# Kernel optimization log

Measured on AMD Instinct MI355X. Metric: run time of the kernel, lower is better.

Reference implementation:

```python
import itertools
import jax, jax.numpy as jnp
import numpy as np

ALPHA = 1e-4   # mse/conn mixing
BETA = 0.1
DMAX = 20.0
NCAP = 10.0    # costs_n_cap
PCAP = 3.0     # costs_p_cap
W3D = 64       # 3D cube window (window_3d)
W2D = 32       # 2D MALIS window (window_2d, default)


def _dilate5(mask):
    # scipy binary_dilation, default cross structuring element, 5 iterations
    m = mask.astype(bool)
    for _ in range(5):
        p = np.pad(m, 1)
        m = p[1:-1, 1:-1] | p[:-2, 1:-1] | p[2:, 1:-1] | p[1:-1, :-2] | p[1:-1, 2:]
    return m


def _label8(mask):
    # skimage.measure.label on boolean mask: 8-connectivity, background=0
    H, W = mask.shape
    lbl = np.zeros((H, W), np.int64)
    parent = {}

    def find(x):
        while parent[x] != x:
            parent[x] = parent[parent[x]]
            x = parent[x]
        return x

    nxt = 1
    for i in range(H):
        for j in range(W):
            if not mask[i, j]:
                continue
            neigh = []
            for di, dj in ((-1, -1), (-1, 0), (-1, 1), (0, -1)):
                ii, jj = i + di, j + dj
                if 0 <= ii < H and 0 <= jj < W and mask[ii, jj]:
                    neigh.append(int(lbl[ii, jj]))
            if not neigh:
                lbl[i, j] = nxt
                parent[nxt] = nxt
                nxt += 1
            else:
                m0 = min(neigh)
                lbl[i, j] = m0
                for nb in neigh:
                    ra, rb = find(m0), find(nb)
                    if ra != rb:
                        parent[max(ra, rb)] = min(ra, rb)
    out = np.zeros_like(lbl)
    remap = {}
    c = 0
    for i in range(H):
        for j in range(W):
            if lbl[i, j] > 0:
                r = find(int(lbl[i, j]))
                if r not in remap:
                    c += 1
                    remap[r] = c
                out[i, j] = remap[r]
    return out


def _malis_edge_weights(seg, n1, n2, costs, pos):
    # MALIS union-find / Kruskal maximal-spanning-tree pair counting.
    # Edges processed in descending cost order. Background (seg==0) nodes
    # are not counted. pos=1: #same-label pairs merged; pos=0: #diff-label pairs.
    n = seg.size
    parent = list(range(n))

    def find(x):
        r = x
        while parent[r] != r:
            r = parent[r]
        while parent[x] != r:
            parent[x], x = r, parent[x]
        return r

    cnt = [({int(s): 1} if s > 0 else {}) for s in seg]
    tot = [1 if s > 0 else 0 for s in seg]
    w = np.zeros(costs.shape[0], np.float32)
    for e in np.argsort(-costs, kind="stable"):
        ra, rb = find(int(n1[e])), find(int(n2[e]))
        if ra == rb:
            continue
        ca, cb = cnt[ra], cnt[rb]
        if len(ca) > len(cb):
            ra, rb, ca, cb = rb, ra, cb, ca
        same = 0
        for l, v in ca.items():
            same += v * cb.get(l, 0)
        w[e] = float(same if pos else tot[ra] * tot[rb] - same)
        for l, v in ca.items():
            cb[l] = cb.get(l, 0) + v
        tot[rb] += tot[ra]
        parent[ra] = rb
        cnt[ra] = None
    return w


def _window_weights(pred2d, tgt2d):
    # numpy MALIS node weights for a [B,1,H,W] 2D projection
    B, C, H, W = pred2d.shape
    w = W2D
    wn = np.zeros(pred2d.shape, np.float32)
    wp = np.zeros(pred2d.shape, np.float32)
    idx = np.arange(w * w).reshape(w, w)
    n1 = np.concatenate([idx[:, :-1].ravel(), idx[:-1, :].ravel()])
    n2 = np.concatenate([idx[:, 1:].ravel(), idx[1:, :].ravel()])
    nh = w * (w - 1)
    for k in range(H // w):
        for j in range(W // w):
            p = pred2d[:, :, k*w:(k+1)*w, j*w:(j+1)*w]
            t = tgt2d[:, :, k*w:(k+1)*w, j*w:(j+1)*w]
            ch = (p[:, :, :, :-1] + p[:, :, :, 1:]).reshape(B, -1)
            cv = (p[:, :, :-1, :] + p[:, :, 1:, :]).reshape(B, -1)
            costs = np.concatenate([ch, cv], 1).astype(np.float32)
            gh = (t[:, :, :, :-1] + t[:, :, :, 1:]).reshape(B, -1)
            gv = (t[:, :, :-1, :] + t[:, :, 1:, :]).reshape(B, -1)
            gt = np.concatenate([gh, gv], 1).astype(np.float32)
            costs_n = costs.copy()
            costs_p = costs.copy()
            costs_n[gt > NCAP] = NCAP
            costs_p[gt < PCAP] = 0.0
            gt = np.minimum(gt, NCAP)
            for b in range(B):
                sg = _label8(~_dilate5(t[b, 0] == 0)).ravel()
                en = _malis_edge_weights(sg, n1, n2, costs_n[b], 0)
                ep = _malis_edge_weights(sg, n1, n2, costs_p[b], 1)
                sn = en.sum()
                if sn > 0:
                    en = en / sn
                sp = ep.sum()
                if sp > 0:
                    ep = ep / sp
                en[gt[b] >= PCAP] = 0.0
                ep[gt[b] < NCAP] = 0.0
                for ew, out in ((en, wn), (ep, wp)):
                    eh = ew[:nh].reshape(w, w - 1)
                    ev = ew[nh:].reshape(w - 1, w)
                    nwt = np.zeros((w, w), np.float32)
                    nwt[:, :-1] += eh
                    nwt[:, 1:] += eh
                    nwt[:-1, :] += ev
                    nwt[1:, :] += ev
                    out[b, 0, k*w:(k+1)*w, j*w:(j+1)*w] = nwt
    return wn, wp


def _precompute(pred_np, tgt_np):
    # host-side (detached) MALIS weight maps, exactly as the torch module
    B, C, H, W, D = pred_np.shape
    items = []
    for k, j, i in itertools.product(range(H // W3D), range(W // W3D), range(D // W3D)):
        sl = (slice(None), slice(None), slice(k*W3D, (k+1)*W3D),
              slice(j*W3D, (j+1)*W3D), slice(i*W3D, (i+1)*W3D))
        pc, tc = pred_np[sl], tgt_np[sl]
        for axis in (2, 3, 4):
            wn, wp = _window_weights(pc.min(axis=axis), tc.min(axis=axis))
            items.append((k, j, i, axis, jnp.asarray(wn), jnp.asarray(wp)))
    return items


def _loss(pred, target, items):
    mse = jnp.mean((pred - target) ** 2)
    conn = jnp.float32(0.0)
    for (k, j, i, axis, wn, wp) in items:
        pc = pred[:, :, k*W3D:(k+1)*W3D, j*W3D:(j+1)*W3D, i*W3D:(i+1)*W3D]
        proj = jnp.min(pc, axis=axis)  # [B,1,64,64]
        conn = conn + jnp.sum(proj**2 * wn + BETA * (DMAX - proj)**2 * wp)
    return (mse, jnp.float32(ALPHA) * conn)


def setup_inputs() -> dict:
    # synthetic distance-transform-like volumes (zeros on 'vessel' seeds)
    rng = np.random.default_rng(0)
    B, H = 4, 128
    g = np.arange(H, dtype=np.float32)
    zz, yy, xx = np.meshgrid(g, g, g, indexing="ij")
    tgt = np.empty((B, 1, H, H, H), np.float32)
    for b in range(B):
        pts = rng.uniform(0, H, size=(24, 3)).astype(np.float32)
        d = np.full((H, H, H), np.inf, np.float32)
        for p in pts:
            d = np.minimum(d, np.sqrt((zz - p[0])**2 + (yy - p[1])**2 + (xx - p[2])**2))
        tgt[b, 0] = np.floor(np.minimum(d, DMAX))
    pred = np.clip(tgt + 0.5 * rng.standard_normal(tgt.shape).astype(np.float32), 0.0, DMAX).astype(np.float32)
    return {"pred": jnp.asarray(pred), "target": jnp.asarray(tgt)}


def reference(pred, target):
    items = _precompute(np.asarray(pred), np.asarray(target))
    return _loss(pred, target, items)
```

## Files before the change

kernel.cpp:

```cpp
#include <hip/hip_runtime.h>

#define BLOCK 256
#define NNODE 1024
#define NH    992
#define NE    1984
#define NSORT 2048
#define LMAX  12
#define CHUNK 64
#define NPASS (NE / CHUNK)

typedef unsigned long long ull;

__device__ __forceinline__ void edge_nodes(int e, int& a, int& b) {
    if (e < NH) {
        int r = e / 31;
        int c = e - r * 31;
        a = (r << 5) + c;
        b = a + 1;
    } else {
        a = e - NH;
        b = a + 32;
    }
}

__device__ __forceinline__ int find_par(unsigned short* par, int x) {
    volatile unsigned short* vp = par;
    int r = x;
    int p = vp[r];
    while (p != r) { r = p; p = vp[r]; }
    int c = x;
    while (c != r) { const int nxt = vp[c]; vp[c] = (unsigned short)r; c = nxt; }
    return r;
}

__device__ __forceinline__ int dot16x4(ull a, ull b) {
    int s  = (int)(a & 0xFFFFu)         * (int)(b & 0xFFFFu);
    s     += (int)((a >> 16) & 0xFFFFu) * (int)((b >> 16) & 0xFFFFu);
    s     += (int)((a >> 32) & 0xFFFFu) * (int)((b >> 32) & 0xFFFFu);
    s     += (int)((a >> 48) & 0xFFFFu) * (int)((b >> 48) & 0xFFFFu);
    return s;
}

__device__ __forceinline__ void cswap(unsigned int& ka, unsigned short& ia,
                                      unsigned int& kb, unsigned short& ib, bool up) {
    const bool gt = (ka > kb) || (ka == kb && ia > ib);
    if (gt == up) {
        const unsigned int  tk = ka; ka = kb; kb = tk;
        const unsigned short ti = ia; ia = ib; ib = ti;
    }
}

__global__ __launch_bounds__(BLOCK) void conn_kernel(const float* __restrict__ pred,
                                                     const float* __restrict__ tgt,
                                                     double* __restrict__ acc_ws,
                                                     int B) {
    __shared__ alignas(16) float          sh_p[NNODE];
    __shared__ alignas(16) float          sh_t[NNODE];
    __shared__ alignas(16) unsigned int   sh_key[NSORT];
    __shared__ alignas(16) unsigned short sh_idx[NSORT];
    __shared__ unsigned short sh_parent[NNODE];
    __shared__ unsigned int   sh_szto[NNODE];
    __shared__ ull            sh_cnt64[NNODE * 3];
    __shared__ unsigned char  sh_seg[NNODE];
    __shared__ int            sh_flag;
    __shared__ int            sh_L;
    __shared__ float          sh_sn;
    __shared__ double         sh_red[4];

    const int tid = threadIdx.x;
    int wg = blockIdx.x;
    const int sign = (wg >> 3) & 1;
    wg = (wg & 7) | ((wg >> 4) << 3);
    const int b    = wg % B;  wg /= B;
    const int win  = wg & 3;  wg >>= 2;
    const int item = wg;
    const int axis_id = item % 3;
    const int cube = item / 3;
    const int ci = cube & 1;
    const int cj = (cube >> 1) & 1;
    const int ck = (cube >> 2) & 1;
    const int wk = win >> 1;
    const int wj = win & 1;

    const size_t base = (size_t)b * 2097152u;

    if (axis_id == 2) {
        for (int pix = tid; pix < NNODE; pix += BLOCK) {
            const int r = pix >> 5, c = pix & 31;
            const int R = wk * 32 + r, C = wj * 32 + c;
            const size_t idx0 = base + (size_t)(ck * 64 + R) * 16384u + (size_t)(cj * 64 + C) * 128u + (size_t)(ci * 64);
            const float4* pp = reinterpret_cast<const float4*>(pred + idx0);
            const float4* tp = reinterpret_cast<const float4*>(tgt + idx0);
            float pm = 3.4e38f, tm = 3.4e38f;
            #pragma unroll
            for (int h = 0; h < 16; ++h) {
                const float4 a = pp[h];
                const float4 t = tp[h];
                pm = fminf(pm, fminf(fminf(a.x, a.y), fminf(a.z, a.w)));
                tm = fminf(tm, fminf(fminf(t.x, t.y), fminf(t.z, t.w)));
            }
            sh_p[pix] = pm;
            sh_t[pix] = tm;
        }
    } else {
        const int r  = tid >> 3;
        const int c0 = (tid & 7) << 2;
        const int R = wk * 32 + r, C = wj * 32 + c0;
        size_t idx0; int hstride;
        if (axis_id == 0) {
            idx0 = base + (size_t)(ck * 64) * 16384u + (size_t)(cj * 64 + R) * 128u + (size_t)(ci * 64 + C);
            hstride = 16384;
        } else {
            idx0 = base + (size_t)(ck * 64 + R) * 16384u + (size_t)(cj * 64) * 128u + (size_t)(ci * 64 + C);
            hstride = 128;
        }
        float4 pm = make_float4(3.4e38f, 3.4e38f, 3.4e38f, 3.4e38f);
        float4 tm = pm;
        #pragma unroll 8
        for (int h = 0; h < 64; ++h) {
            const float4 a  = *reinterpret_cast<const float4*>(pred + idx0);
            const float4 t4 = *reinterpret_cast<const float4*>(tgt + idx0);
            pm.x = fminf(pm.x, a.x);  pm.y = fminf(pm.y, a.y);
            pm.z = fminf(pm.z, a.z);  pm.w = fminf(pm.w, a.w);
            tm.x = fminf(tm.x, t4.x); tm.y = fminf(tm.y, t4.y);
            tm.z = fminf(tm.z, t4.z); tm.w = fminf(tm.w, t4.w);
            idx0 += (size_t)hstride;
        }
        *reinterpret_cast<float4*>(&sh_p[(r << 5) + c0]) = pm;
        *reinterpret_cast<float4*>(&sh_t[(r << 5) + c0]) = tm;
    }
    __syncthreads();

    unsigned char* mA = sh_seg;
    unsigned char* mB = (unsigned char*)sh_idx;
    for (int pix = tid; pix < NNODE; pix += BLOCK)
        mA[pix] = (sh_t[pix] == 0.0f) ? 1 : 0;
    __syncthreads();
    for (int it = 0; it < 5; ++it) {
        unsigned char* src = (it & 1) ? mB : mA;
        unsigned char* dst = (it & 1) ? mA : mB;
        for (int pix = tid; pix < NNODE; pix += BLOCK) {
            const int r = pix >> 5, c = pix & 31;
            unsigned char v = src[pix];
            if (r > 0)  v |= src[pix - 32];
            if (r < 31) v |= src[pix + 32];
            if (c > 0)  v |= src[pix - 1];
            if (c < 31) v |= src[pix + 1];
            dst[pix] = v;
        }
        __syncthreads();
    }
    for (int pix = tid; pix < NNODE; pix += BLOCK)
        mA[pix] = mB[pix] ^ 1;
    __syncthreads();

    for (int pix = tid; pix < NNODE; pix += BLOCK)
        sh_parent[pix] = mA[pix] ? (unsigned short)pix : (unsigned short)0xFFFF;
    __syncthreads();
    for (;;) {
        if (tid == 0) sh_flag = 0;
        __syncthreads();
        for (int pix = tid; pix < NNODE; pix += BLOCK) {
            if (!mA[pix]) continue;
            const int r = pix >> 5, c = pix & 31;
            int m = sh_parent[pix];
            #pragma unroll
            for (int d = 0; d < 8; ++d) {
                static const int dr[8] = {-1,-1,-1, 0, 0, 1, 1, 1};
                static const int dc[8] = {-1, 0, 1,-1, 1,-1, 0, 1};
                const int rr = r + dr[d], cc = c + dc[d];
                if (rr < 0 || rr > 31 || cc < 0 || cc > 31) continue;
                const int nb = (rr << 5) + cc;
                if (mA[nb]) { int v = sh_parent[nb]; if (v < m) m = v; }
            }
            while ((int)sh_parent[m] < m) m = sh_parent[m];
            if (m < (int)sh_parent[pix]) { sh_parent[pix] = (unsigned short)m; sh_flag = 1; }
        }
        __syncthreads();
        const int f = sh_flag;
        __syncthreads();
        if (f == 0) break;
    }

    if (tid == 0) sh_L = 0;
    __syncthreads();
    for (int pix = tid; pix < NNODE; pix += BLOCK) {
        if (mA[pix] && (int)sh_parent[pix] == pix) {
            const int id = atomicAdd(&sh_L, 1);
            sh_szto[pix] = (unsigned int)(id + 1);
        }
    }
    __syncthreads();
    for (int pix = tid; pix < NNODE; pix += BLOCK) {
        unsigned char s = 0;
        if (mA[pix]) {
            int lab = (int)sh_szto[sh_parent[pix]];
            if (lab > 255) lab = 255;
            s = (unsigned char)lab;
        }
        sh_seg[pix] = s;
    }
    __syncthreads();

    for (int pix = tid; pix < NNODE; pix += BLOCK) {
        sh_parent[pix] = (unsigned short)pix;
        const int s = sh_seg[pix];
        const unsigned int tot = (s > 0 && s <= LMAX) ? 1u : 0u;
        sh_szto[pix] = 1u | (tot << 16);
        ull c0 = 0, c1 = 0, c2 = 0;
        if (s >= 1 && s <= LMAX) {
            const ull bit = 1ull << (((s - 1) & 3) * 16);
            const int q = (s - 1) >> 2;
            if (q == 0) c0 = bit; else if (q == 1) c1 = bit; else c2 = bit;
        }
        sh_cnt64[pix * 3 + 0] = c0;
        sh_cnt64[pix * 3 + 1] = c1;
        sh_cnt64[pix * 3 + 2] = c2;
    }
    __syncthreads();

    unsigned int   K[8];
    unsigned short I[8];
    const int b8 = tid << 3;
    #pragma unroll
    for (int l = 0; l < 8; ++l) {
        const int e = b8 + l;
        if (e < NE) {
            int a, bb; edge_nodes(e, a, bb);
            float cost = sh_p[a] + sh_p[bb];
            const float g = sh_t[a] + sh_t[bb];
            if (sign == 0) { if (g > 10.0f) cost = 10.0f; }
            else           { if (g <  3.0f) cost = 0.0f;  }
            K[l] = ~__float_as_uint(cost);
            I[l] = (unsigned short)e;
        } else {
            K[l] = 0xFFFFFFFFu;
            I[l] = (unsigned short)0xFFFF;
        }
    }
    cswap(K[0],I[0],K[1],I[1], true );
    cswap(K[2],I[2],K[3],I[3], false);
    cswap(K[4],I[4],K[5],I[5], true );
    cswap(K[6],I[6],K[7],I[7], false);
    cswap(K[0],I[0],K[2],I[2], true );
    cswap(K[1],I[1],K[3],I[3], true );
    cswap(K[4],I[4],K[6],I[6], false);
    cswap(K[5],I[5],K[7],I[7], false);
    cswap(K[0],I[0],K[1],I[1], true );
    cswap(K[2],I[2],K[3],I[3], true );
    cswap(K[4],I[4],K[5],I[5], false);
    cswap(K[6],I[6],K[7],I[7], false);
    {
        const bool u8 = ((b8 & 8) == 0);
        cswap(K[0],I[0],K[4],I[4], u8); cswap(K[1],I[1],K[5],I[5], u8);
        cswap(K[2],I[2],K[6],I[6], u8); cswap(K[3],I[3],K[7],I[7], u8);
        cswap(K[0],I[0],K[2],I[2], u8); cswap(K[1],I[1],K[3],I[3], u8);
        cswap(K[4],I[4],K[6],I[6], u8); cswap(K[5],I[5],K[7],I[7], u8);
        cswap(K[0],I[0],K[1],I[1], u8); cswap(K[2],I[2],K[3],I[3], u8);
        cswap(K[4],I[4],K[5],I[5], u8); cswap(K[6],I[6],K[7],I[7], u8);
    }
    {
        uint4 k0, k1, iv;
        k0.x=K[0]; k0.y=K[1]; k0.z=K[2]; k0.w=K[3];
        k1.x=K[4]; k1.y=K[5]; k1.z=K[6]; k1.w=K[7];
        iv.x=(unsigned int)I[0] | ((unsigned int)I[1]<<16);
        iv.y=(unsigned int)I[2] | ((unsigned int)I[3]<<16);
        iv.z=(unsigned int)I[4] | ((unsigned int)I[5]<<16);
        iv.w=(unsigned int)I[6] | ((unsigned int)I[7]<<16);
        *reinterpret_cast<uint4*>(&sh_key[b8])     = k0;
        *reinterpret_cast<uint4*>(&sh_key[b8 + 4]) = k1;
        *reinterpret_cast<uint4*>(&sh_idx[b8])     = iv;
    }
    __syncthreads();

    for (int k = 16; k <= NSORT; k <<= 1) {
        for (int j = k >> 1; j >= 8; j >>= 1) {
            for (int p = tid; p < (NSORT >> 1); p += BLOCK) {
                const int i   = ((p & ~(j - 1)) << 1) | (p & (j - 1));
                const int ixj = i | j;
                const unsigned int ka = sh_key[i], kb = sh_key[ixj];
                const unsigned short ia = sh_idx[i], ib = sh_idx[ixj];
                const bool gt = (ka > kb) || (ka == kb && ia > ib);
                const bool up = ((i & k) == 0);
                if (gt == up) {
                    sh_key[i] = kb; sh_key[ixj] = ka;
                    sh_idx[i] = ib; sh_idx[ixj] = ia;
                }
            }
            __syncthreads();
        }
        {
            const uint4 k0 = *reinterpret_cast<const uint4*>(&sh_key[b8]);
            const uint4 k1 = *reinterpret_cast<const uint4*>(&sh_key[b8 + 4]);
            const uint4 iv = *reinterpret_cast<const uint4*>(&sh_idx[b8]);
            K[0]=k0.x; K[1]=k0.y; K[2]=k0.z; K[3]=k0.w;
            K[4]=k1.x; K[5]=k1.y; K[6]=k1.z; K[7]=k1.w;
            I[0]=(unsigned short)(iv.x); I[1]=(unsigned short)(iv.x>>16);
            I[2]=(unsigned short)(iv.y); I[3]=(unsigned short)(iv.y>>16);
            I[4]=(unsigned short)(iv.z); I[5]=(unsigned short)(iv.z>>16);
            I[6]=(unsigned short)(iv.w); I[7]=(unsigned short)(iv.w>>16);
            const bool u8 = ((b8 & k) == 0);
            cswap(K[0],I[0],K[4],I[4], u8); cswap(K[1],I[1],K[5],I[5], u8);
            cswap(K[2],I[2],K[6],I[6], u8); cswap(K[3],I[3],K[7],I[7], u8);
            cswap(K[0],I[0],K[2],I[2], u8); cswap(K[1],I[1],K[3],I[3], u8);
            cswap(K[4],I[4],K[6],I[6], u8); cswap(K[5],I[5],K[7],I[7], u8);
            cswap(K[0],I[0],K[1],I[1], u8); cswap(K[2],I[2],K[3],I[3], u8);
            cswap(K[4],I[4],K[5],I[5], u8); cswap(K[6],I[6],K[7],I[7], u8);
            uint4 o0, o1, ov;
            o0.x=K[0]; o0.y=K[1]; o0.z=K[2]; o0.w=K[3];
            o1.x=K[4]; o1.y=K[5]; o1.z=K[6]; o1.w=K[7];
            ov.x=(unsigned int)I[0] | ((unsigned int)I[1]<<16);
            ov.y=(unsigned int)I[2] | ((unsigned int)I[3]<<16);
            ov.z=(unsigned int)I[4] | ((unsigned int)I[5]<<16);
            ov.w=(unsigned int)I[6] | ((unsigned int)I[7]<<16);
            *reinterpret_cast<uint4*>(&sh_key[b8])     = o0;
            *reinterpret_cast<uint4*>(&sh_key[b8 + 4]) = o1;
            *reinterpret_cast<uint4*>(&sh_idx[b8])     = ov;
        }
        __syncthreads();
    }

    for (int e = tid; e < NE; e += BLOCK) sh_key[e] = 0u;
    __syncthreads();

    if (tid < 64) {
        const int lane = tid;
        for (int pass = 0; pass < NPASS; ++pass) {
            const int e = sh_idx[pass * CHUNK + lane];
            int a, bb; edge_nodes(e, a, bb);
            int ra = find_par(sh_parent, a);
            int rb = find_par(sh_parent, bb);
            ull m = __ballot(ra != rb);
            if (m == 0) continue;
            int i0 = (int)__builtin_ctzll(m); m &= m - 1;
            unsigned int pk = (unsigned int)__shfl(
                (int)((unsigned int)ra | ((unsigned int)rb << 10) | ((unsigned int)e << 20)), i0);
            for (;;) {
                const int ra_i = (int)(pk & 1023u);
                const int rb_i = (int)((pk >> 10) & 1023u);
                const bool live = (ra_i != rb_i);
                unsigned int xa = 0, xb = 0;
                ull a0 = 0, a1 = 0, a2 = 0, b0 = 0, b1 = 0, b2 = 0;
                if (live) {
                    xa = sh_szto[ra_i]; xb = sh_szto[rb_i];
                    a0 = sh_cnt64[ra_i * 3 + 0];
                    a1 = sh_cnt64[ra_i * 3 + 1];
                    a2 = sh_cnt64[ra_i * 3 + 2];
                    b0 = sh_cnt64[rb_i * 3 + 0];
                    b1 = sh_cnt64[rb_i * 3 + 1];
                    b2 = sh_cnt64[rb_i * 3 + 2];
                }
                const bool have_next = (m != 0);
                unsigned int pk_next = 0;
                if (have_next) {
                    const int ni = (int)__builtin_ctzll(m); m &= m - 1;
                    pk_next = (unsigned int)__shfl(
                        (int)((unsigned int)ra | ((unsigned int)rb << 10) | ((unsigned int)e << 20)), ni);
                }
                if (live) {
                    const int ta = (int)(xa >> 16), tb = (int)(xb >> 16);
                    const int same = dot16x4(a0, b0) + dot16x4(a1, b1) + dot16x4(a2, b2);
                    const int wv = sign ? same : (ta * tb - same);
                    const int big = ((xa & 0xFFFFu) > (xb & 0xFFFFu));
                    const int rs = big ? ra_i : rb_i;
                    const int rl = big ? rb_i : ra_i;
                    const int se = (int)(pk >> 20);
                    if (lane == 0) {
                        sh_key[se] = __float_as_uint((float)wv);
                        sh_cnt64[rs * 3 + 0] = a0 + b0;
                        sh_cnt64[rs * 3 + 1] = a1 + b1;
                        sh_cnt64[rs * 3 + 2] = a2 + b2;
                        sh_szto[rs] = xa + xb;
                        sh_parent[rl] = (unsigned short)rs;
                    }
                    if (ra == rl) ra = rs;
                    if (rb == rl) rb = rs;
                    if (have_next) {
                        unsigned int r1 = pk_next & 1023u;
                        unsigned int r2 = (pk_next >> 10) & 1023u;
                        if (r1 == (unsigned int)rl) r1 = (unsigned int)rs;
                        if (r2 == (unsigned int)rl) r2 = (unsigned int)rs;
                        pk_next = r1 | (r2 << 10) | (pk_next & 0xFFF00000u);
                    }
                }
                if (!have_next) break;
                pk = pk_next;
            }
        }
    }
    __syncthreads();

    {
        float part = 0.0f;
        for (int e = tid; e < NE; e += BLOCK) part += __uint_as_float(sh_key[e]);
        for (int off = 32; off > 0; off >>= 1) part += __shfl_down(part, off, 64);
        if ((tid & 63) == 0) sh_red[tid >> 6] = (double)part;
        __syncthreads();
        if (tid == 0) sh_sn = (float)(sh_red[0] + sh_red[1] + sh_red[2] + sh_red[3]);
        __syncthreads();
    }
    const float sn = sh_sn;

    double acc = 0.0;
    for (int pix = tid; pix < NNODE; pix += BLOCK) {
        const int r = pix >> 5, c = pix & 31;
        float nw = 0.0f;
        if (c < 31) { const int e = r * 31 + c;
            float v = __uint_as_float(sh_key[e]); if (sn > 0.0f) v = v / sn;
            const float g = sh_t[pix] + sh_t[pix + 1];
            if (sign == 0) { if (g >= 3.0f) v = 0.0f; } else { if (g < 10.0f) v = 0.0f; }
            nw += v; }
        if (c > 0)  { const int e = r * 31 + c - 1;
            float v = __uint_as_float(sh_key[e]); if (sn > 0.0f) v = v / sn;
            const float g = sh_t[pix - 1] + sh_t[pix];
            if (sign == 0) { if (g >= 3.0f) v = 0.0f; } else { if (g < 10.0f) v = 0.0f; }
            nw += v; }
        if (r < 31) { const int e = NH + pix;
            float v = __uint_as_float(sh_key[e]); if (sn > 0.0f) v = v / sn;
            const float g = sh_t[pix] + sh_t[pix + 32];
            if (sign == 0) { if (g >= 3.0f) v = 0.0f; } else { if (g < 10.0f) v = 0.0f; }
            nw += v; }
        if (r > 0)  { const int e = NH + pix - 32;
            float v = __uint_as_float(sh_key[e]); if (sn > 0.0f) v = v / sn;
            const float g = sh_t[pix - 32] + sh_t[pix];
            if (sign == 0) { if (g >= 3.0f) v = 0.0f; } else { if (g < 10.0f) v = 0.0f; }
            nw += v; }
        const float p = sh_p[pix];
        float term;
        if (sign == 0) {
            term = (p * p) * nw;
        } else {
            const float d = 20.0f - p;
            term = (0.1f * (d * d)) * nw;
        }
        acc += (double)term;
    }
    for (int off = 32; off > 0; off >>= 1) acc += __shfl_down(acc, off, 64);
    if ((tid & 63) == 0) sh_red[tid >> 6] = acc;
    __syncthreads();
    if (tid == 0)
        atomicAdd(&acc_ws[1], sh_red[0] + sh_red[1] + sh_red[2] + sh_red[3]);
}

__global__ __launch_bounds__(BLOCK) void mse_kernel(const float* __restrict__ pred,
                                                    const float* __restrict__ tgt,
                                                    double* __restrict__ acc_ws,
                                                    long n) {
    double acc = 0.0;
    for (long i = (long)blockIdx.x * BLOCK + threadIdx.x; i < n; i += (long)gridDim.x * BLOCK) {
        const float d = pred[i] - tgt[i];
        acc += (double)(d * d);
    }
    for (int off = 32; off > 0; off >>= 1) acc += __shfl_down(acc, off, 64);
    __shared__ double red[4];
    if ((threadIdx.x & 63) == 0) red[threadIdx.x >> 6] = acc;
    __syncthreads();
    if (threadIdx.x == 0)
        atomicAdd(&acc_ws[0], red[0] + red[1] + red[2] + red[3]);
}

__global__ void fin_kernel(const double* __restrict__ acc_ws, float* __restrict__ out, long n) {
    if (threadIdx.x == 0 && blockIdx.x == 0) {
        out[0] = (float)(acc_ws[0] / (double)n);
        out[1] = (float)(acc_ws[1] * (double)1e-4f);
    }
}

extern "C" void kernel_launch(void* const* d_in, const int* in_sizes, int n_in,
                              void* d_out, int out_size, void* d_ws, size_t ws_size,
                              hipStream_t stream) {
    const float* pred = (const float*)d_in[0];
    const float* tgt  = (const float*)d_in[1];
    float* out = (float*)d_out;
    double* acc = (double*)d_ws;

    const long n = (long)in_sizes[0];
    const int  B = (int)(n / 2097152);

    hipMemsetAsync(d_ws, 0, 2 * sizeof(double), stream);
    mse_kernel<<<1024, BLOCK, 0, stream>>>(pred, tgt, acc, n);
    conn_kernel<<<192 * B, BLOCK, 0, stream>>>(pred, tgt, acc, B);
    fin_kernel<<<1, 64, 0, stream>>>(acc, out, n);
}
```

Measured before the change: 562.6 us.

## Process non-conflicting union-find merges in parallel across wavefront lanes

Replaces the serial one-edge-at-a-time Kruskal merge loop with a conflict-graph scheme. Each chunk of 64 edges builds a per-lane conflict mask from shared root IDs. All lanes whose lower-indexed pending edges do not conflict then merge at once, after which the conflict sets are expanded and roots are re-resolved. This aims to cut the serial dependency chain of the MALIS merge phase. The cost is an O(P) shuffle loop to build conflicts, extra ballots per round, and repeated find_par calls, which may not pay off when chunks are dense with conflicts.

```diff
diff --git a/kernel.cpp b/kernel.cpp
--- a/kernel.cpp
+++ b/kernel.cpp
@@ -325,66 +325,67 @@
 
     if (tid < 64) {
         const int lane = tid;
+        const ull below = (lane == 0) ? 0ull : (~0ull >> (64 - lane));
         for (int pass = 0; pass < NPASS; ++pass) {
             const int e = sh_idx[pass * CHUNK + lane];
             int a, bb; edge_nodes(e, a, bb);
             int ra = find_par(sh_parent, a);
             int rb = find_par(sh_parent, bb);
-            ull m = __ballot(ra != rb);
-            if (m == 0) continue;
-            int i0 = (int)__builtin_ctzll(m); m &= m - 1;
-            unsigned int pk = (unsigned int)__shfl(
-                (int)((unsigned int)ra | ((unsigned int)rb << 10) | ((unsigned int)e << 20)), i0);
-            for (;;) {
-                const int ra_i = (int)(pk & 1023u);
-                const int rb_i = (int)((pk >> 10) & 1023u);
-                const bool live = (ra_i != rb_i);
-                unsigned int xa = 0, xb = 0;
-                ull a0 = 0, a1 = 0, a2 = 0, b0 = 0, b1 = 0, b2 = 0;
-                if (live) {
-                    xa = sh_szto[ra_i]; xb = sh_szto[rb_i];
-                    a0 = sh_cnt64[ra_i * 3 + 0];
-                    a1 = sh_cnt64[ra_i * 3 + 1];
-                    a2 = sh_cnt64[ra_i * 3 + 2];
-                    b0 = sh_cnt64[rb_i * 3 + 0];
-                    b1 = sh_cnt64[rb_i * 3 + 1];
-                    b2 = sh_cnt64[rb_i * 3 + 2];
+            ull P = __ballot(ra != rb);
+            if (P == 0) continue;
+            ull conf = 0;
+            {
+                const unsigned int mypack = (unsigned int)ra | ((unsigned int)rb << 10);
+                ull t = P;
+                while (t) {
+                    const int j = (int)__builtin_ctzll(t); t &= t - 1;
+                    const unsigned int o = (unsigned int)__shfl((int)mypack, j);
+                    const int ora = (int)(o & 1023u), orb = (int)((o >> 10) & 1023u);
+                    if (ra == ora || ra == orb || rb == ora || rb == orb)
+                        conf |= (1ull << j);
                 }
-                const bool have_next = (m != 0);
-                unsigned int pk_next = 0;
-                if (have_next) {
-                    const int ni = (int)__builtin_ctzll(m); m &= m - 1;
-                    pk_next = (unsigned int)__shfl(
-                        (int)((unsigned int)ra | ((unsigned int)rb << 10) | ((unsigned int)e << 20)), ni);
-                }
-                if (live) {
+            }
+            while (P) {
+                const bool mine = ((P >> lane) & 1ull) != 0ull;
+                const bool ok = mine && ((conf & P & below) == 0ull);
+                const ull S = __ballot(ok);
+                if (ok) {
+                    const unsigned int xa = sh_szto[ra], xb = sh_szto[rb];
+                    const ull a0 = sh_cnt64[ra * 3 + 0];
+                    const ull a1 = sh_cnt64[ra * 3 + 1];
+                    const ull a2 = sh_cnt64[ra * 3 + 2];
+                    const ull b0 = sh_cnt64[rb * 3 + 0];
+                    const ull b1 = sh_cnt64[rb * 3 + 1];
+                    const ull b2 = sh_cnt64[rb * 3 + 2];
                     const int ta = (int)(xa >> 16), tb = (int)(xb >> 16);
                     const int same = dot16x4(a0, b0) + dot16x4(a1, b1) + dot16x4(a2, b2);
                     const int wv = sign ? same : (ta * tb - same);
                     const int big = ((xa & 0xFFFFu) > (xb & 0xFFFFu));
-                    const int rs = big ? ra_i : rb_i;
-                    const int rl = big ? rb_i : ra_i;
-                    const int se = (int)(pk >> 20);
-                    if (lane == 0) {
-                        sh_key[se] = __float_as_uint((float)wv);
-                        sh_cnt64[rs * 3 + 0] = a0 + b0;
-                        sh_cnt64[rs * 3 + 1] = a1 + b1;
-                        sh_cnt64[rs * 3 + 2] = a2 + b2;
-                        sh_szto[rs] = xa + xb;
-                        sh_parent[rl] = (unsigned short)rs;
-                    }
-                    if (ra == rl) ra = rs;
-                    if (rb == rl) rb = rs;
-                    if (have_next) {
-                        unsigned int r1 = pk_next & 1023u;
-                        unsigned int r2 = (pk_next >> 10) & 1023u;
-                        if (r1 == (unsigned int)rl) r1 = (unsigned int)rs;
-                        if (r2 == (unsigned int)rl) r2 = (unsigned int)rs;
-                        pk_next = r1 | (r2 << 10) | (pk_next & 0xFFF00000u);
-                    }
+                    const int rs = big ? ra : rb;
+                    const int rl = big ? rb : ra;
+                    sh_key[e] = __float_as_uint((float)wv);
+                    sh_cnt64[rs * 3 + 0] = a0 + b0;
+                    sh_cnt64[rs * 3 + 1] = a1 + b1;
+                    sh_cnt64[rs * 3 + 2] = a2 + b2;
+                    sh_szto[rs] = xa + xb;
+                    sh_parent[rl] = (unsigned short)rs;
                 }
-                if (!have_next) break;
-                pk = pk_next;
+                asm volatile("s_waitcnt lgkmcnt(0)" ::: "memory");
+                __builtin_amdgcn_sched_barrier(0);
+                ull s2 = S;
+                while (s2) {
+                    const int j = (int)__builtin_ctzll(s2); s2 &= s2 - 1;
+                    const bool withj = ((conf >> j) & 1ull) != 0ull;
+                    const ull Cj = __ballot(withj);
+                    if (withj) conf |= Cj;
+                }
+                P &= ~S;
+                const bool alive = ((P >> lane) & 1ull) != 0ull;
+                if (alive) {
+                    ra = find_par(sh_parent, ra);
+                    rb = find_par(sh_parent, rb);
+                }
+                P = __ballot(alive && ra != rb);
             }
         }
     }
```

New measurement: 845.3 us. 1.5x slower.

## Specialize MALIS union-find by label count and skip windows with no labels

Applied to the files above, without the earlier changes.

Counts the connected-component labels in each window and chooses one of three modes. Windows with no labels, or with a single label in the negative pass, skip all the MALIS work. Windows with few labels keep only one 64-bit count word per node, and the one-label case needs no counts at all. The merge loop is also simplified: it drops the software-pipelined prefetch of the next pack and re-shuffles inside a plain while loop, and it skips count updates when both roots carry zero labelled nodes. The aim is less shared-memory traffic and fewer serial union steps. The risk is a longer serial dependency per merge, since the next pack is no longer fetched early.

```diff
diff --git a/kernel.cpp b/kernel.cpp
--- a/kernel.cpp
+++ b/kernel.cpp
@@ -202,20 +202,30 @@
     }
     __syncthreads();
 
+    const int Lraw = sh_L;
+    const int mode = (Lraw <= 1) ? 0 : ((Lraw <= 4) ? 1 : 2);
+    const bool skip_all = (Lraw == 0) || (Lraw == 1 && sign == 0);
+
+    if (!skip_all) {
+
     for (int pix = tid; pix < NNODE; pix += BLOCK) {
         sh_parent[pix] = (unsigned short)pix;
         const int s = sh_seg[pix];
         const unsigned int tot = (s > 0 && s <= LMAX) ? 1u : 0u;
         sh_szto[pix] = 1u | (tot << 16);
-        ull c0 = 0, c1 = 0, c2 = 0;
-        if (s >= 1 && s <= LMAX) {
-            const ull bit = 1ull << (((s - 1) & 3) * 16);
-            const int q = (s - 1) >> 2;
-            if (q == 0) c0 = bit; else if (q == 1) c1 = bit; else c2 = bit;
-        }
-        sh_cnt64[pix * 3 + 0] = c0;
-        sh_cnt64[pix * 3 + 1] = c1;
-        sh_cnt64[pix * 3 + 2] = c2;
+        if (mode >= 1) {
+            ull c0 = 0, c1 = 0, c2 = 0;
+            if (s >= 1 && s <= LMAX) {
+                const ull bit = 1ull << (((s - 1) & 3) * 16);
+                const int q = (s - 1) >> 2;
+                if (q == 0) c0 = bit; else if (q == 1) c1 = bit; else c2 = bit;
+            }
+            sh_cnt64[pix * 3 + 0] = c0;
+            if (mode == 2) {
+                sh_cnt64[pix * 3 + 1] = c1;
+                sh_cnt64[pix * 3 + 2] = c2;
+            }
+        }
     }
     __syncthreads();
 
@@ -331,60 +341,52 @@
             int ra = find_par(sh_parent, a);
             int rb = find_par(sh_parent, bb);
             ull m = __ballot(ra != rb);
-            if (m == 0) continue;
-            int i0 = (int)__builtin_ctzll(m); m &= m - 1;
-            unsigned int pk = (unsigned int)__shfl(
-                (int)((unsigned int)ra | ((unsigned int)rb << 10) | ((unsigned int)e << 20)), i0);
-            for (;;) {
+            while (m) {
+                const int i = (int)__builtin_ctzll(m);
+                m &= m - 1;
+                const unsigned int pack = (unsigned int)ra | ((unsigned int)rb << 10) | ((unsigned int)e << 20);
+                const unsigned int pk = (unsigned int)__shfl((int)pack, i);
                 const int ra_i = (int)(pk & 1023u);
                 const int rb_i = (int)((pk >> 10) & 1023u);
-                const bool live = (ra_i != rb_i);
-                unsigned int xa = 0, xb = 0;
-                ull a0 = 0, a1 = 0, a2 = 0, b0 = 0, b1 = 0, b2 = 0;
-                if (live) {
-                    xa = sh_szto[ra_i]; xb = sh_szto[rb_i];
-                    a0 = sh_cnt64[ra_i * 3 + 0];
-                    a1 = sh_cnt64[ra_i * 3 + 1];
-                    a2 = sh_cnt64[ra_i * 3 + 2];
-                    b0 = sh_cnt64[rb_i * 3 + 0];
-                    b1 = sh_cnt64[rb_i * 3 + 1];
-                    b2 = sh_cnt64[rb_i * 3 + 2];
-                }
-                const bool have_next = (m != 0);
-                unsigned int pk_next = 0;
-                if (have_next) {
-                    const int ni = (int)__builtin_ctzll(m); m &= m - 1;
-                    pk_next = (unsigned int)__shfl(
-                        (int)((unsigned int)ra | ((unsigned int)rb << 10) | ((unsigned int)e << 20)), ni);
-                }
-                if (live) {
-                    const int ta = (int)(xa >> 16), tb = (int)(xb >> 16);
+                if (ra_i == rb_i) continue;
+                const int se = (int)(pk >> 20);
+                const unsigned int xa = sh_szto[ra_i], xb = sh_szto[rb_i];
+                const int ta = (int)(xa >> 16), tb = (int)(xb >> 16);
+                const int big = ((xa & 0xFFFFu) > (xb & 0xFFFFu));
+                const int rs = big ? ra_i : rb_i;
+                const int rl = big ? rb_i : ra_i;
+                int wv;
+                if (mode == 0) {
+                    wv = ta * tb;
+                } else if (mode == 1) {
+                    const ull a0 = sh_cnt64[ra_i * 3];
+                    const ull b0 = sh_cnt64[rb_i * 3];
+                    const int same = dot16x4(a0, b0);
+                    wv = sign ? same : (ta * tb - same);
+                    if (lane == 0 && (ta + tb) > 0)
+                        sh_cnt64[rs * 3] = a0 + b0;
+                } else {
+                    const ull a0 = sh_cnt64[ra_i * 3 + 0];
+                    const ull a1 = sh_cnt64[ra_i * 3 + 1];
+                    const ull a2 = sh_cnt64[ra_i * 3 + 2];
+                    const ull b0 = sh_cnt64[rb_i * 3 + 0];
+                    const ull b1 = sh_cnt64[rb_i * 3 + 1];
+                    const ull b2 = sh_cnt64[rb_i * 3 + 2];
                     const int same = dot16x4(a0, b0) + dot16x4(a1, b1) + dot16x4(a2, b2);
-                    const int wv = sign ? same : (ta * tb - same);
-                    const int big = ((xa & 0xFFFFu) > (xb & 0xFFFFu));
-                    const int rs = big ? ra_i : rb_i;
-                    const int rl = big ? rb_i : ra_i;
-                    const int se = (int)(pk >> 20);
-                    if (lane == 0) {
-                        sh_key[se] = __float_as_uint((float)wv);
+                    wv = sign ? same : (ta * tb - same);
+                    if (lane == 0 && (ta + tb) > 0) {
                         sh_cnt64[rs * 3 + 0] = a0 + b0;
                         sh_cnt64[rs * 3 + 1] = a1 + b1;
                         sh_cnt64[rs * 3 + 2] = a2 + b2;
-                        sh_szto[rs] = xa + xb;
-                        sh_parent[rl] = (unsigned short)rs;
-                    }
-                    if (ra == rl) ra = rs;
-                    if (rb == rl) rb = rs;
-                    if (have_next) {
-                        unsigned int r1 = pk_next & 1023u;
-                        unsigned int r2 = (pk_next >> 10) & 1023u;
-                        if (r1 == (unsigned int)rl) r1 = (unsigned int)rs;
-                        if (r2 == (unsigned int)rl) r2 = (unsigned int)rs;
-                        pk_next = r1 | (r2 << 10) | (pk_next & 0xFFF00000u);
                     }
                 }
-                if (!have_next) break;
-                pk = pk_next;
+                if (lane == 0) {
+                    sh_key[se] = __float_as_uint((float)wv);
+                    sh_szto[rs] = xa + xb;
+                    sh_parent[rl] = (unsigned short)rs;
+                }
+                if (ra == rl) ra = rs;
+                if (rb == rl) rb = rs;
             }
         }
     }
@@ -440,6 +442,8 @@
     __syncthreads();
     if (tid == 0)
         atomicAdd(&acc_ws[1], sh_red[0] + sh_red[1] + sh_red[2] + sh_red[3]);
+
+    }
 }
 
 __global__ __launch_bounds__(BLOCK) void mse_kernel(const float* __restrict__ pred,
```

Measured after the change: 530.7 us. 5.7% less time.
